# Performance work log

Hardware: AMD Instinct MI355X
Metric: run time of the kernel (lower is better)

## Reference

```python
import jax, jax.numpy as jnp
import numpy as np

N = 100_000
E = 1_000_000
D = 64
NORM_FACTOR = 100.0
LN_EPS = 1e-5


def setup_inputs() -> dict:
    key = jax.random.key(0)
    ks = jax.random.split(key, 8)
    h = jax.random.normal(ks[0], (N, D), dtype=jnp.float32)
    distances = jax.random.uniform(ks[1], (E, 1), dtype=jnp.float32)
    edges = jax.random.randint(ks[2], (2, E), 0, N, dtype=jnp.int64)
    node_mask = jnp.ones((N, 1), dtype=jnp.float32)
    edge_mask = jnp.ones((E, 1), dtype=jnp.float32)
    s = 1.0 / np.sqrt(D)
    W_lin = jax.random.normal(ks[3], (D, D), dtype=jnp.float32) * s
    b_lin = jnp.zeros((D,), dtype=jnp.float32)
    att_W1 = jax.random.normal(ks[4], (D, 2 * D + 1), dtype=jnp.float32) * (1.0 / np.sqrt(2 * D + 1))
    att_b1 = jnp.zeros((D,), dtype=jnp.float32)
    att_W2 = jax.random.normal(ks[5], (1, D), dtype=jnp.float32) * s
    att_b2 = jnp.zeros((1,), dtype=jnp.float32)
    ln_g = jnp.ones((D,), dtype=jnp.float32)
    ln_b = jnp.zeros((D,), dtype=jnp.float32)
    return {"h": h, "distances": distances, "edges": edges, "node_mask": node_mask,
            "edge_mask": edge_mask, "W_lin": W_lin, "b_lin": b_lin,
            "att_W1": att_W1, "att_b1": att_b1, "att_W2": att_W2, "att_b2": att_b2,
            "ln_g": ln_g, "ln_b": ln_b}


def reference(h, distances, edges, node_mask, edge_mask, W_lin, b_lin,
              att_W1, att_b1, att_W2, att_b2, ln_g, ln_b):
    # Linear projection: [N, D]
    x = h @ W_lin.T + b_lin
    row, col = edges[0], edges[1]
    x_row = x[row]          # [E, D]
    x_col = x[col]          # [E, D]
    # DenseAtt: MLP(concat(x_row, x_col, dist)) -> sigmoid -> * edge_mask
    cat = jnp.concatenate([x_row, x_col, distances], axis=1)  # [E, 2D+1]
    hdn = jax.nn.silu(cat @ att_W1.T + att_b1)                # [E, D]
    att = jax.nn.sigmoid(hdn @ att_W2.T + att_b2) * edge_mask # [E, 1]
    # Attention-weighted scatter-sum aggregation into row segments
    agg = x_col * att
    out = jax.ops.segment_sum(agg, row, num_segments=x.shape[0]) / NORM_FACTOR
    out = out + x           # residual
    # LayerNorm + activation
    mu = jnp.mean(out, axis=-1, keepdims=True)
    var = jnp.mean(jnp.square(out - mu), axis=-1, keepdims=True)
    y = (out - mu) * jax.lax.rsqrt(var + LN_EPS) * ln_g + ln_b
    return jax.nn.silu(y)
```

## Files before the change

kernel.cpp:

```cpp
#include <hip/hip_runtime.h>
#include <hip/hip_bf16.h>

#define N_NODES 100000
#define N_EDGES 1000000
#define DIM 64
#define NORM_INV 0.01f
#define LN_EPS 1e-5f
#define N_TILES 6250
#define PROJ_BLOCKS 1563
#define N_BUCKETS 1563
#define HB_PK 784
#define SC_EDGES 4096
#define SC_BLOCKS 245
#define OFS_STRIDE 1568
#define L2E 1.4426950408889634f
#define LN2 0.6931471805599453f
#define CAP 1280

typedef __attribute__((ext_vector_type(8))) short short8;
typedef __attribute__((ext_vector_type(4))) float f32x4;

__device__ __forceinline__ unsigned short f2bf(float f) {
    union { float f; unsigned u; } x; x.f = f;
    unsigned r = x.u + 0x7FFFu + ((x.u >> 16) & 1u);
    return (unsigned short)(r >> 16);
}
__device__ __forceinline__ float bf2f(unsigned short s) {
    union { unsigned u; float f; } x; x.u = ((unsigned)s) << 16; return x.f;
}

__global__ __launch_bounds__(256) void scatter_k(
    const int* __restrict__ edges, const float* __restrict__ dist,
    const float* __restrict__ emask,
    uint2* __restrict__ srec, unsigned short* __restrict__ ofsT) {
    __shared__ __align__(16) char pool[39040];
    __shared__ int wsum[4];
    int* lh = (int*)pool;
    int* lofsP = (int*)pool + HB_PK;
    uint2* lsort = (uint2*)(pool + 6272);
    const int blk = blockIdx.x;
    const int tid = threadIdx.x;
    const int lane = tid & 63;
    const int w = tid >> 6;
    for (int i = tid; i < HB_PK; i += 256) lh[i] = 0;
    __syncthreads();

    const int eb = blk * SC_EDGES;
    const int total = min(SC_EDGES, N_EDGES - eb);

    int rows[16], rank[16];
    uint2 recs[16];
    const int e0 = eb + tid * 16;
#pragma unroll
    for (int g = 0; g < 4; ++g) {
        const int e = e0 + g * 4;
        if (e + 4 <= N_EDGES) {
            const int4 rr = *(const int4*)(edges + e);
            const int4 cc = *(const int4*)(edges + N_EDGES + e);
            const float4 dd = *(const float4*)(dist + e);
            const float4 mm = *(const float4*)(emask + e);
            rows[g*4+0] = rr.x; rows[g*4+1] = rr.y; rows[g*4+2] = rr.z; rows[g*4+3] = rr.w;
            const int c4[4] = {cc.x, cc.y, cc.z, cc.w};
            const float d4[4] = {dd.x, dd.y, dd.z, dd.w};
            const float m4[4] = {mm.x, mm.y, mm.z, mm.w};
#pragma unroll
            for (int i = 0; i < 4; ++i) {
                const int ii = g * 4 + i;
                recs[ii].x = (unsigned)c4[i] | ((unsigned)(rows[ii] & 63) << 24);
                recs[ii].y = (unsigned)f2bf(d4[i]) |
                             ((unsigned)f2bf(m4[i] * NORM_INV) << 16);
                const int bk = rows[ii] >> 6;
                const int sh = (bk & 1) << 4;
                rank[ii] = (atomicAdd(&lh[bk >> 1], 1 << sh) >> sh) & 0xffff;
            }
        } else {
#pragma unroll
            for (int i = 0; i < 4; ++i) {
                const int ii = g * 4 + i;
                const int ee = e + i;
                if (ee < N_EDGES) {
                    rows[ii] = edges[ee];
                    recs[ii].x = (unsigned)edges[N_EDGES + ee] |
                                 ((unsigned)(rows[ii] & 63) << 24);
                    recs[ii].y = (unsigned)f2bf(dist[ee]) |
                                 ((unsigned)f2bf(emask[ee] * NORM_INV) << 16);
                    const int bk = rows[ii] >> 6;
                    const int sh = (bk & 1) << 4;
                    rank[ii] = (atomicAdd(&lh[bk >> 1], 1 << sh) >> sh) & 0xffff;
                } else {
                    rows[ii] = -1;
                }
            }
        }
    }
    __syncthreads();

    const int t4 = tid * 4;
    int li[4];
#pragma unroll
    for (int g = 0; g < 4; ++g) li[g] = (t4 + g < HB_PK) ? lh[t4 + g] : 0;
    int cs[8];
#pragma unroll
    for (int g = 0; g < 4; ++g) {
        cs[2*g]   = li[g] & 0xffff;
        cs[2*g+1] = (li[g] >> 16) & 0xffff;
    }
    int S = 0;
#pragma unroll
    for (int k = 0; k < 8; ++k) S += cs[k];
    int sc = S;
#pragma unroll
    for (int off = 1; off < 64; off <<= 1) {
        int u = __shfl_up(sc, off);
        if (lane >= off) sc += u;
    }
    if (lane == 63) wsum[w] = sc;
    __syncthreads();
    int wbase = 0;
    if (w > 0) wbase = wsum[0];
    if (w > 1) wbase += wsum[1];
    if (w > 2) wbase += wsum[2];
    int run = sc - S + wbase;
#pragma unroll
    for (int g = 0; g < 4; ++g) {
        const int lo = run; run += cs[2*g];
        const int hi = run; run += cs[2*g+1];
        if (t4 + g < HB_PK) lofsP[t4 + g] = (unsigned)lo | ((unsigned)hi << 16);
    }
    __syncthreads();

#pragma unroll
    for (int i = 0; i < 16; ++i) {
        if (rows[i] >= 0) {
            const int bk = rows[i] >> 6;
            const int base = (lofsP[bk >> 1] >> ((bk & 1) << 4)) & 0xffff;
            lsort[base + rank[i]] = recs[i];
        }
    }
    __syncthreads();

    for (int s = tid; s < total; s += 256)
        srec[(size_t)blk * SC_EDGES + s] = lsort[s];
    for (int b = tid; b < 1564; b += 256)
        ofsT[blk * OFS_STRIDE + b] =
            (unsigned short)((lofsP[b >> 1] >> ((b & 1) << 4)) & 0xffff);
}

__global__ __launch_bounds__(256) void proj_k(
    const float* __restrict__ h, const float* __restrict__ bl,
    const float* __restrict__ W, const float* __restrict__ att_W1,
    unsigned short* __restrict__ xv, unsigned short* __restrict__ u_bf) {
    __shared__ __align__(16) char pool[32768];

    const int tid = threadIdx.x;
    const int lane = tid & 63;
    const int wv = tid >> 6;
    const int c = lane & 15, q = lane >> 4;

    {
        short8* Lwhi_w = (short8*)pool;
        short8* Lwlo_w = Lwhi_w + 512;
        short8* Lwa_w  = Lwhi_w + 1024;
        short8* Lwb_w  = Lwhi_w + 1536;
        const int nt_b = tid >> 6;
        const int n_b = nt_b * 16 + c;
#pragma unroll
        for (int ks = 0; ks < 2; ++ks) {
            const int k0 = ks * 32 + q * 8;
            short8 hi8, lo8, a8, b8;
#pragma unroll
            for (int jj = 0; jj < 8; ++jj) {
                float w = W[n_b * 64 + k0 + jj];
                unsigned short hh = f2bf(w);
                hi8[jj] = (short)hh;
                lo8[jj] = (short)f2bf(w - bf2f(hh));
                a8[jj] = (short)f2bf(att_W1[n_b * 129 + k0 + jj]);
                b8[jj] = (short)f2bf(att_W1[n_b * 129 + 64 + k0 + jj]);
            }
            const int idx = (nt_b * 2 + ks) * 64 + lane;
            Lwhi_w[idx] = hi8; Lwlo_w[idx] = lo8; Lwa_w[idx] = a8; Lwb_w[idx] = b8;
        }
    }
    __syncthreads();
    const short8* Lwhi = (const short8*)pool;
    const short8* Lwlo = Lwhi + 512;
    const short8* Lwa  = Lwhi + 1024;
    const short8* Lwb  = Lwhi + 1536;

    const int tile = blockIdx.x * 4 + wv;
    const bool valid = (tile < N_TILES);
    const int n0 = valid ? tile * 16 : 0;

    float bias[4];
#pragma unroll
    for (int nt = 0; nt < 4; ++nt) bias[nt] = bl[nt * 16 + c];

    short8 Ahi[2], Alo[2];
#pragma unroll
    for (int ks = 0; ks < 2; ++ks) {
        const float* hp = h + (size_t)(n0 + c) * 64 + ks * 32 + q * 8;
        f32x4 p0 = *(const f32x4*)hp;
        f32x4 p1 = *(const f32x4*)(hp + 4);
        short8 hi8, lo8;
#pragma unroll
        for (int jj = 0; jj < 4; ++jj) {
            unsigned short hh = f2bf(p0[jj]);
            hi8[jj] = (short)hh; lo8[jj] = (short)f2bf(p0[jj] - bf2f(hh));
            unsigned short h2 = f2bf(p1[jj]);
            hi8[4 + jj] = (short)h2; lo8[4 + jj] = (short)f2bf(p1[jj] - bf2f(h2));
        }
        Ahi[ks] = hi8; Alo[ks] = lo8;
    }

    f32x4 xacc[4] = {{0,0,0,0},{0,0,0,0},{0,0,0,0},{0,0,0,0}};
#pragma unroll
    for (int ks = 0; ks < 2; ++ks)
#pragma unroll
        for (int nt = 0; nt < 4; ++nt) {
            const short8 fhi = Lwhi[(nt * 2 + ks) * 64 + lane];
            const short8 flo = Lwlo[(nt * 2 + ks) * 64 + lane];
            xacc[nt] = __builtin_amdgcn_mfma_f32_16x16x32_bf16(Ahi[ks], fhi, xacc[nt], 0, 0, 0);
            xacc[nt] = __builtin_amdgcn_mfma_f32_16x16x32_bf16(Ahi[ks], flo, xacc[nt], 0, 0, 0);
            xacc[nt] = __builtin_amdgcn_mfma_f32_16x16x32_bf16(Alo[ks], fhi, xacc[nt], 0, 0, 0);
        }

    __syncthreads();

    unsigned short* lw = (unsigned short*)pool + wv * (16 * 72);
    uint2 xpk[4];
#pragma unroll
    for (int r = 0; r < 4; ++r) {
        unsigned short xb[4];
#pragma unroll
        for (int nt = 0; nt < 4; ++nt) {
            unsigned short v16 = f2bf(xacc[nt][r] + bias[nt]);
            xb[nt] = v16;
            lw[(q * 4 + r) * 72 + nt * 16 + c] = v16;
        }
        xpk[r].x = (unsigned)xb[0] | ((unsigned)xb[1] << 16);
        xpk[r].y = (unsigned)xb[2] | ((unsigned)xb[3] << 16);
    }

    short8 Ax[2];
#pragma unroll
    for (int ks = 0; ks < 2; ++ks)
        Ax[ks] = *(const short8*)&lw[c * 72 + ks * 32 + q * 8];

    f32x4 uacc[4] = {{0,0,0,0},{0,0,0,0},{0,0,0,0},{0,0,0,0}};
    f32x4 vacc[4] = {{0,0,0,0},{0,0,0,0},{0,0,0,0},{0,0,0,0}};
#pragma unroll
    for (int ks = 0; ks < 2; ++ks)
#pragma unroll
        for (int nt = 0; nt < 4; ++nt) {
            const short8 fa = Lwa[(nt * 2 + ks) * 64 + lane];
            const short8 fb = Lwb[(nt * 2 + ks) * 64 + lane];
            uacc[nt] = __builtin_amdgcn_mfma_f32_16x16x32_bf16(Ax[ks], fa, uacc[nt], 0, 0, 0);
            vacc[nt] = __builtin_amdgcn_mfma_f32_16x16x32_bf16(Ax[ks], fb, vacc[nt], 0, 0, 0);
        }
    if (valid) {
#pragma unroll
        for (int r = 0; r < 4; ++r) {
            const int node = n0 + q * 4 + r;
            uint2 pu;
            pu.x = (unsigned)f2bf(uacc[0][r] * L2E) | ((unsigned)f2bf(uacc[1][r] * L2E) << 16);
            pu.y = (unsigned)f2bf(uacc[2][r] * L2E) | ((unsigned)f2bf(uacc[3][r] * L2E) << 16);
            *(uint2*)(u_bf + (size_t)node * 64 + c * 4) = pu;
            uint4 pk;
            pk.x = xpk[r].x;
            pk.y = xpk[r].y;
            pk.z = (unsigned)f2bf(vacc[0][r] * L2E) | ((unsigned)f2bf(vacc[1][r] * L2E) << 16);
            pk.w = (unsigned)f2bf(vacc[2][r] * L2E) | ((unsigned)f2bf(vacc[3][r] * L2E) << 16);
            *(uint4*)(xv + (size_t)node * 128 + c * 8) = pk;
        }
    }
}

__global__ __launch_bounds__(256, 8) void agg_fused(
    const uint2* __restrict__ srec, const unsigned short* __restrict__ ofsT,
    const unsigned short* __restrict__ xv, const unsigned short* __restrict__ u_bf,
    const float* __restrict__ att_W1, const float* __restrict__ att_b1,
    const float* __restrict__ att_W2, const float* __restrict__ att_b2,
    const float* __restrict__ ln_g, const float* __restrict__ ln_b,
    float* __restrict__ out) {
    __shared__ __align__(16) uint2 lrecs[CAP + 16];
    __shared__ float4 ltab[64];
    __shared__ int hist[64];
    __shared__ int rst[65];
    __shared__ int cur[64];
    __shared__ int sst[256];
    __shared__ int dbase[257];
    __shared__ int wsum4[4];

    const int b = blockIdx.x;
    const int tid = threadIdx.x;
    const int lane = tid & 63;
    const int wv = tid >> 6;

    if (tid < 64) hist[tid] = 0;
    if (tid >= 192) {
        const int f = tid - 192;
        ltab[f] = make_float4(att_W2[f] * LN2, att_W1[f * 129 + 128] * L2E,
                              att_b1[f] * L2E, 0.f);
    }

    int stv = 0, len = 0, sc0 = 0;
    {
        if (tid < SC_BLOCKS) {
            stv = (int)ofsT[tid * OFS_STRIDE + b];
            len = (int)ofsT[tid * OFS_STRIDE + b + 1] - stv;
        }
        sst[tid] = stv;
        sc0 = len;
#pragma unroll
        for (int off = 1; off < 64; off <<= 1) {
            int u = __shfl_up(sc0, off);
            if (lane >= off) sc0 += u;
        }
        if (lane == 63) wsum4[wv] = sc0;
    }
    __syncthreads();
    {
        int wbase = 0;
        if (wv > 0) wbase = wsum4[0];
        if (wv > 1) wbase += wsum4[1];
        if (wv > 2) wbase += wsum4[2];
        dbase[tid] = wbase + sc0 - len;
        if (tid == 255) dbase[256] = wbase + sc0;
    }
    __syncthreads();
    const int cnt = dbase[245];

    uint2 rec0, rec1, rec2, rec3;
    int lr0 = -1, lr1 = -1, lr2 = -1, lr3 = -1;
#define GATHER(I, RC, LR)                                                     \
    {                                                                         \
        const int m = tid + I * 256;                                          \
        if (m < cnt) {                                                        \
            int lo = 0, hi = 245;                                             \
            while (hi - lo > 1) {                                             \
                const int mid = (lo + hi) >> 1;                               \
                if (dbase[mid] <= m) lo = mid; else hi = mid;                 \
            }                                                                 \
            RC = srec[(size_t)lo * SC_EDGES + sst[lo] + (m - dbase[lo])];     \
            LR = (int)(RC.x >> 24);                                           \
            RC.x &= 0x00FFFFFFu;                                              \
            atomicAdd(&hist[LR], 1);                                          \
        }                                                                     \
    }
    GATHER(0, rec0, lr0)
    GATHER(1, rec1, lr1)
    GATHER(2, rec2, lr2)
    GATHER(3, rec3, lr3)
#undef GATHER
    __syncthreads();

    if (tid < 64) {
        const int c = hist[tid];
        const int p = (c + 3) & ~3;
        int sc = p;
#pragma unroll
        for (int off = 1; off < 64; off <<= 1) {
            int u = __shfl_up(sc, off);
            if (lane >= off) sc += u;
        }
        const int excl = sc - p;
        rst[tid] = excl;
        cur[tid] = excl;
        uint2 z; z.x = 0; z.y = 0;
        for (int i = c; i < p; ++i) lrecs[excl + i] = z;
        if (tid == 63) {
            rst[64] = excl + p;
            for (int i = 0; i < 16; ++i) lrecs[excl + p + i] = z;
        }
    }
    __syncthreads();

    if (lr0 >= 0) lrecs[atomicAdd(&cur[lr0], 1)] = rec0;
    if (lr1 >= 0) lrecs[atomicAdd(&cur[lr1], 1)] = rec1;
    if (lr2 >= 0) lrecs[atomicAdd(&cur[lr2], 1)] = rec2;
    if (lr3 >= 0) lrecs[atomicAdd(&cur[lr3], 1)] = rec3;
    __syncthreads();

    const int j = lane & 15;
    const int sl = lane >> 4;
    const float4 t0 = ltab[j], t1 = ltab[j + 16], t2 = ltab[j + 32], t3 = ltab[j + 48];
    const float b2L = att_b2[0] * L2E;
    const float gg = ln_g[lane], bb = ln_b[lane];
    const unsigned* xvu = (const unsigned*)xv;

#pragma unroll 1
    for (int k = 0; k < 16; ++k) {
        const int lrw = wv + 4 * k;
        const int r = b * 64 + lrw;
        if (r >= N_NODES) break;

        const uint2 uu = *(const uint2*)(u_bf + (size_t)r * 64 + j * 4);
        const float base0 = __uint_as_float(uu.x << 16) + t0.z;
        const float base1 = __uint_as_float(uu.x & 0xffff0000u) + t1.z;
        const float base2 = __uint_as_float(uu.y << 16) + t2.z;
        const float base3 = __uint_as_float(uu.y & 0xffff0000u) + t3.z;

        const int s0 = rst[lrw];
        const int e1 = rst[lrw + 1];

        float a0 = 0.f, a1 = 0.f, a2 = 0.f, a3 = 0.f;
        if (e1 > s0) {
            uint2 recA = lrecs[s0 + sl];
            uint2 recB = lrecs[s0 + 4 + sl];
            uint4 xvA = *(const uint4*)(xvu + (size_t)recA.x * 64 + j * 4);
            uint4 xvB = *(const uint4*)(xvu + (size_t)recB.x * 64 + j * 4);
            for (int e = s0; e < e1; e += 4) {
                const uint2 recC = lrecs[e + 8 + sl];
                const uint4 xvC = *(const uint4*)(xvu + (size_t)recC.x * 64 + j * 4);

                const float dist = __uint_as_float(recA.y << 16);
                const float emN = __uint_as_float(recA.y & 0xffff0000u);
                const float x0 = __uint_as_float(xvA.x << 16);
                const float x1 = __uint_as_float(xvA.x & 0xffff0000u);
                const float x2 = __uint_as_float(xvA.y << 16);
                const float x3 = __uint_as_float(xvA.y & 0xffff0000u);
                const float v0 = __uint_as_float(xvA.z << 16);
                const float v1 = __uint_as_float(xvA.z & 0xffff0000u);
                const float v2 = __uint_as_float(xvA.w << 16);
                const float v3 = __uint_as_float(xvA.w & 0xffff0000u);
                float pv = 0.f, pre, sg;
                pre = fmaf(dist, t0.y, base0) + v0;
                sg = __builtin_amdgcn_rcpf(1.f + __builtin_amdgcn_exp2f(-pre));
                pv = fmaf(pre * sg, t0.x, pv);
                pre = fmaf(dist, t1.y, base1) + v1;
                sg = __builtin_amdgcn_rcpf(1.f + __builtin_amdgcn_exp2f(-pre));
                pv = fmaf(pre * sg, t1.x, pv);
                pre = fmaf(dist, t2.y, base2) + v2;
                sg = __builtin_amdgcn_rcpf(1.f + __builtin_amdgcn_exp2f(-pre));
                pv = fmaf(pre * sg, t2.x, pv);
                pre = fmaf(dist, t3.y, base3) + v3;
                sg = __builtin_amdgcn_rcpf(1.f + __builtin_amdgcn_exp2f(-pre));
                pv = fmaf(pre * sg, t3.x, pv);
                pv += __shfl_xor(pv, 1); pv += __shfl_xor(pv, 2);
                pv += __shfl_xor(pv, 4); pv += __shfl_xor(pv, 8);
                const float sp = fmaf(pv, L2E, b2L);
                const float att =
                    emN * __builtin_amdgcn_rcpf(1.f + __builtin_amdgcn_exp2f(-sp));
                a0 = fmaf(att, x0, a0); a1 = fmaf(att, x1, a1);
                a2 = fmaf(att, x2, a2); a3 = fmaf(att, x3, a3);
                recA = recB; xvA = xvB; recB = recC; xvB = xvC;
            }
        }
        a0 += __shfl_xor(a0, 16); a0 += __shfl_xor(a0, 32);
        a1 += __shfl_xor(a1, 16); a1 += __shfl_xor(a1, 32);
        a2 += __shfl_xor(a2, 16); a2 += __shfl_xor(a2, 32);
        a3 += __shfl_xor(a3, 16); a3 += __shfl_xor(a3, 32);

        const uint2 xr = *(const uint2*)(xvu + (size_t)r * 64 + j * 4);
        const float o0 = __uint_as_float(xr.x << 16) + a0;
        const float o1 = __uint_as_float(xr.x & 0xffff0000u) + a1;
        const float o2 = __uint_as_float(xr.y << 16) + a2;
        const float o3 = __uint_as_float(xr.y & 0xffff0000u) + a3;

        float ssum = o0 + o1 + o2 + o3;
        ssum += __shfl_xor(ssum, 1); ssum += __shfl_xor(ssum, 2);
        ssum += __shfl_xor(ssum, 4); ssum += __shfl_xor(ssum, 8);
        const float mu = ssum * (1.f / 64.f);
        const float d0 = o0 - mu, d1 = o1 - mu, d2 = o2 - mu, d3 = o3 - mu;
        float vs = d0 * d0 + d1 * d1 + d2 * d2 + d3 * d3;
        vs += __shfl_xor(vs, 1); vs += __shfl_xor(vs, 2);
        vs += __shfl_xor(vs, 4); vs += __shfl_xor(vs, 8);
        const float rstd = rsqrtf(vs * (1.f / 64.f) + LN_EPS);

        const float dk = (sl == 0) ? d0 : (sl == 1) ? d1 : (sl == 2) ? d2 : d3;
        const float y = fmaf(dk * rstd, gg, bb);
        out[(size_t)r * 64 + lane] =
            y * __builtin_amdgcn_rcpf(1.f + __builtin_amdgcn_exp2f(-y * L2E));
    }
}

extern "C" void kernel_launch(void* const* d_in, const int* in_sizes, int n_in,
                              void* d_out, int out_size, void* d_ws, size_t ws_size,
                              hipStream_t stream) {
    const float* h      = (const float*)d_in[0];
    const float* dist   = (const float*)d_in[1];
    const int*   edges  = (const int*)d_in[2];
    const float* emask  = (const float*)d_in[4];
    const float* W_lin  = (const float*)d_in[5];
    const float* b_lin  = (const float*)d_in[6];
    const float* att_W1 = (const float*)d_in[7];
    const float* att_b1 = (const float*)d_in[8];
    const float* att_W2 = (const float*)d_in[9];
    const float* att_b2 = (const float*)d_in[10];
    const float* ln_g   = (const float*)d_in[11];
    const float* ln_b   = (const float*)d_in[12];
    float* out = (float*)d_out;

    char* ws = (char*)d_ws;
    unsigned short* xv   = (unsigned short*)ws;
    unsigned short* u_bf = (unsigned short*)(ws + 25600000);
    uint2* srec          = (uint2*)(ws + 38400000);
    unsigned short* ofsT = (unsigned short*)(ws + 46428160);

    scatter_k<<<SC_BLOCKS, 256, 0, stream>>>(edges, dist, emask, srec, ofsT);
    proj_k<<<PROJ_BLOCKS, 256, 0, stream>>>(h, b_lin, W_lin, att_W1, xv, u_bf);
    agg_fused<<<N_BUCKETS, 256, 0, stream>>>(srec, ofsT, xv, u_bf,
                                             att_W1, att_b1, att_W2, att_b2,
                                             ln_g, ln_b, out);
}
```

Baseline: 197.2 us.

## Merge scatter and projection into one launch and split aggregation launch

```diff
diff --git a/kernel.cpp b/kernel.cpp
--- a/kernel.cpp
+++ b/kernel.cpp
@@ -9,6 +9,8 @@
 #define N_TILES 6250
 #define PROJ_BLOCKS 1563
 #define N_BUCKETS 1563
+#define AGG_C0 782
+#define AGG_C1 781
 #define HB_PK 784
 #define SC_EDGES 4096
 #define SC_BLOCKS 245
@@ -29,128 +31,128 @@
     union { unsigned u; float f; } x; x.u = ((unsigned)s) << 16; return x.f;
 }
 
-__global__ __launch_bounds__(256) void scatter_k(
+__global__ __launch_bounds__(256) void proj_scatter(
+    const float* __restrict__ h, const float* __restrict__ bl,
+    const float* __restrict__ W, const float* __restrict__ att_W1,
     const int* __restrict__ edges, const float* __restrict__ dist,
     const float* __restrict__ emask,
-    uint2* __restrict__ srec, unsigned short* __restrict__ ofsT) {
-    __shared__ __align__(16) char pool[39040];
+    uint2* __restrict__ srec, unsigned short* __restrict__ ofsT,
+    unsigned short* __restrict__ xv, unsigned short* __restrict__ u_bf) {
+    __shared__ __align__(16) char pool[39168];
     __shared__ int wsum[4];
-    int* lh = (int*)pool;
-    int* lofsP = (int*)pool + HB_PK;
-    uint2* lsort = (uint2*)(pool + 6272);
-    const int blk = blockIdx.x;
-    const int tid = threadIdx.x;
-    const int lane = tid & 63;
-    const int w = tid >> 6;
-    for (int i = tid; i < HB_PK; i += 256) lh[i] = 0;
-    __syncthreads();
-
-    const int eb = blk * SC_EDGES;
-    const int total = min(SC_EDGES, N_EDGES - eb);
-
-    int rows[16], rank[16];
-    uint2 recs[16];
-    const int e0 = eb + tid * 16;
-#pragma unroll
-    for (int g = 0; g < 4; ++g) {
-        const int e = e0 + g * 4;
-        if (e + 4 <= N_EDGES) {
-            const int4 rr = *(const int4*)(edges + e);
-            const int4 cc = *(const int4*)(edges + N_EDGES + e);
-            const float4 dd = *(const float4*)(dist + e);
-            const float4 mm = *(const float4*)(emask + e);
-            rows[g*4+0] = rr.x; rows[g*4+1] = rr.y; rows[g*4+2] = rr.z; rows[g*4+3] = rr.w;
-            const int c4[4] = {cc.x, cc.y, cc.z, cc.w};
-            const float d4[4] = {dd.x, dd.y, dd.z, dd.w};
-            const float m4[4] = {mm.x, mm.y, mm.z, mm.w};
-#pragma unroll
-            for (int i = 0; i < 4; ++i) {
-                const int ii = g * 4 + i;
-                recs[ii].x = (unsigned)c4[i] | ((unsigned)(rows[ii] & 63) << 24);
-                recs[ii].y = (unsigned)f2bf(d4[i]) |
-                             ((unsigned)f2bf(m4[i] * NORM_INV) << 16);
-                const int bk = rows[ii] >> 6;
-                const int sh = (bk & 1) << 4;
-                rank[ii] = (atomicAdd(&lh[bk >> 1], 1 << sh) >> sh) & 0xffff;
-            }
-        } else {
-#pragma unroll
-            for (int i = 0; i < 4; ++i) {
-                const int ii = g * 4 + i;
-                const int ee = e + i;
-                if (ee < N_EDGES) {
-                    rows[ii] = edges[ee];
-                    recs[ii].x = (unsigned)edges[N_EDGES + ee] |
-                                 ((unsigned)(rows[ii] & 63) << 24);
-                    recs[ii].y = (unsigned)f2bf(dist[ee]) |
-                                 ((unsigned)f2bf(emask[ee] * NORM_INV) << 16);
+
+    if (blockIdx.x < SC_BLOCKS) {
+        int* lh = (int*)pool;
+        int* lofsP = (int*)pool + HB_PK;
+        uint2* lsort = (uint2*)(pool + 6272);
+        const int blk = blockIdx.x;
+        const int tid = threadIdx.x;
+        const int lane = tid & 63;
+        const int w = tid >> 6;
+        for (int i = tid; i < HB_PK; i += 256) lh[i] = 0;
+        __syncthreads();
+
+        const int eb = blk * SC_EDGES;
+        const int total = min(SC_EDGES, N_EDGES - eb);
+
+        int rows[16], rank[16];
+        uint2 recs[16];
+        const int e0 = eb + tid * 16;
+#pragma unroll
+        for (int g = 0; g < 4; ++g) {
+            const int e = e0 + g * 4;
+            if (e + 4 <= N_EDGES) {
+                const int4 rr = *(const int4*)(edges + e);
+                const int4 cc = *(const int4*)(edges + N_EDGES + e);
+                const float4 dd = *(const float4*)(dist + e);
+                const float4 mm = *(const float4*)(emask + e);
+                rows[g*4+0] = rr.x; rows[g*4+1] = rr.y; rows[g*4+2] = rr.z; rows[g*4+3] = rr.w;
+                const int c4[4] = {cc.x, cc.y, cc.z, cc.w};
+                const float d4[4] = {dd.x, dd.y, dd.z, dd.w};
+                const float m4[4] = {mm.x, mm.y, mm.z, mm.w};
+#pragma unroll
+                for (int i = 0; i < 4; ++i) {
+                    const int ii = g * 4 + i;
+                    recs[ii].x = (unsigned)c4[i] | ((unsigned)(rows[ii] & 63) << 24);
+                    recs[ii].y = (unsigned)f2bf(d4[i]) |
+                                 ((unsigned)f2bf(m4[i] * NORM_INV) << 16);
                     const int bk = rows[ii] >> 6;
                     const int sh = (bk & 1) << 4;
                     rank[ii] = (atomicAdd(&lh[bk >> 1], 1 << sh) >> sh) & 0xffff;
-                } else {
-                    rows[ii] = -1;
+                }
+            } else {
+#pragma unroll
+                for (int i = 0; i < 4; ++i) {
+                    const int ii = g * 4 + i;
+                    const int ee = e + i;
+                    if (ee < N_EDGES) {
+                        rows[ii] = edges[ee];
+                        recs[ii].x = (unsigned)edges[N_EDGES + ee] |
+                                     ((unsigned)(rows[ii] & 63) << 24);
+                        recs[ii].y = (unsigned)f2bf(dist[ee]) |
+                                     ((unsigned)f2bf(emask[ee] * NORM_INV) << 16);
+                        const int bk = rows[ii] >> 6;
+                        const int sh = (bk & 1) << 4;
+                        rank[ii] = (atomicAdd(&lh[bk >> 1], 1 << sh) >> sh) & 0xffff;
+                    } else {
+                        rows[ii] = -1;
+                    }
                 }
             }
         }
-    }
-    __syncthreads();
-
-    const int t4 = tid * 4;
-    int li[4];
-#pragma unroll
-    for (int g = 0; g < 4; ++g) li[g] = (t4 + g < HB_PK) ? lh[t4 + g] : 0;
-    int cs[8];
-#pragma unroll
-    for (int g = 0; g < 4; ++g) {
-        cs[2*g]   = li[g] & 0xffff;
-        cs[2*g+1] = (li[g] >> 16) & 0xffff;
-    }
-    int S = 0;
-#pragma unroll
-    for (int k = 0; k < 8; ++k) S += cs[k];
-    int sc = S;
-#pragma unroll
-    for (int off = 1; off < 64; off <<= 1) {
-        int u = __shfl_up(sc, off);
-        if (lane >= off) sc += u;
-    }
-    if (lane == 63) wsum[w] = sc;
-    __syncthreads();
-    int wbase = 0;
-    if (w > 0) wbase = wsum[0];
-    if (w > 1) wbase += wsum[1];
-    if (w > 2) wbase += wsum[2];
-    int run = sc - S + wbase;
-#pragma unroll
-    for (int g = 0; g < 4; ++g) {
-        const int lo = run; run += cs[2*g];
-        const int hi = run; run += cs[2*g+1];
-        if (t4 + g < HB_PK) lofsP[t4 + g] = (unsigned)lo | ((unsigned)hi << 16);
-    }
-    __syncthreads();
-
-#pragma unroll
-    for (int i = 0; i < 16; ++i) {
-        if (rows[i] >= 0) {
-            const int bk = rows[i] >> 6;
-            const int base = (lofsP[bk >> 1] >> ((bk & 1) << 4)) & 0xffff;
-            lsort[base + rank[i]] = recs[i];
-        }
-    }
-    __syncthreads();
-
-    for (int s = tid; s < total; s += 256)
-        srec[(size_t)blk * SC_EDGES + s] = lsort[s];
-    for (int b = tid; b < 1564; b += 256)
-        ofsT[blk * OFS_STRIDE + b] =
-            (unsigned short)((lofsP[b >> 1] >> ((b & 1) << 4)) & 0xffff);
-}
-
-__global__ __launch_bounds__(256) void proj_k(
-    const float* __restrict__ h, const float* __restrict__ bl,
-    const float* __restrict__ W, const float* __restrict__ att_W1,
-    unsigned short* __restrict__ xv, unsigned short* __restrict__ u_bf) {
-    __shared__ __align__(16) char pool[32768];
+        __syncthreads();
+
+        const int t4 = tid * 4;
+        int li[4];
+#pragma unroll
+        for (int g = 0; g < 4; ++g) li[g] = (t4 + g < HB_PK) ? lh[t4 + g] : 0;
+        int cs[8];
+#pragma unroll
+        for (int g = 0; g < 4; ++g) {
+            cs[2*g]   = li[g] & 0xffff;
+            cs[2*g+1] = (li[g] >> 16) & 0xffff;
+        }
+        int S = 0;
+#pragma unroll
+        for (int k = 0; k < 8; ++k) S += cs[k];
+        int sc = S;
+#pragma unroll
+        for (int off = 1; off < 64; off <<= 1) {
+            int u = __shfl_up(sc, off);
+            if (lane >= off) sc += u;
+        }
+        if (lane == 63) wsum[w] = sc;
+        __syncthreads();
+        int wbase = 0;
+        if (w > 0) wbase = wsum[0];
+        if (w > 1) wbase += wsum[1];
+        if (w > 2) wbase += wsum[2];
+        int run = sc - S + wbase;
+#pragma unroll
+        for (int g = 0; g < 4; ++g) {
+            const int lo = run; run += cs[2*g];
+            const int hi = run; run += cs[2*g+1];
+            if (t4 + g < HB_PK) lofsP[t4 + g] = (unsigned)lo | ((unsigned)hi << 16);
+        }
+        __syncthreads();
+
+#pragma unroll
+        for (int i = 0; i < 16; ++i) {
+            if (rows[i] >= 0) {
+                const int bk = rows[i] >> 6;
+                const int base = (lofsP[bk >> 1] >> ((bk & 1) << 4)) & 0xffff;
+                lsort[base + rank[i]] = recs[i];
+            }
+        }
+        __syncthreads();
+
+        for (int s = tid; s < total; s += 256)
+            srec[(size_t)blk * SC_EDGES + s] = lsort[s];
+        for (int b = tid; b < 1564; b += 256)
+            ofsT[blk * OFS_STRIDE + b] =
+                (unsigned short)((lofsP[b >> 1] >> ((b & 1) << 4)) & 0xffff);
+        return;
+    }
 
     const int tid = threadIdx.x;
     const int lane = tid & 63;
@@ -187,7 +189,7 @@
     const short8* Lwa  = Lwhi + 1024;
     const short8* Lwb  = Lwhi + 1536;
 
-    const int tile = blockIdx.x * 4 + wv;
+    const int tile = (blockIdx.x - SC_BLOCKS) * 4 + wv;
     const bool valid = (tile < N_TILES);
     const int n0 = valid ? tile * 16 : 0;
 
@@ -281,7 +283,7 @@
     const float* __restrict__ att_W1, const float* __restrict__ att_b1,
     const float* __restrict__ att_W2, const float* __restrict__ att_b2,
     const float* __restrict__ ln_g, const float* __restrict__ ln_b,
-    float* __restrict__ out) {
+    float* __restrict__ out, const int bbase) {
     __shared__ __align__(16) uint2 lrecs[CAP + 16];
     __shared__ float4 ltab[64];
     __shared__ int hist[64];
@@ -291,7 +293,7 @@
     __shared__ int dbase[257];
     __shared__ int wsum4[4];
 
-    const int b = blockIdx.x;
+    const int b = bbase + blockIdx.x;
     const int tid = threadIdx.x;
     const int lane = tid & 63;
     const int wv = tid >> 6;
@@ -413,7 +415,7 @@
                 const uint2 recC = lrecs[e + 8 + sl];
                 const uint4 xvC = *(const uint4*)(xvu + (size_t)recC.x * 64 + j * 4);
 
-                const float dist = __uint_as_float(recA.y << 16);
+                const float dst = __uint_as_float(recA.y << 16);
                 const float emN = __uint_as_float(recA.y & 0xffff0000u);
                 const float x0 = __uint_as_float(xvA.x << 16);
                 const float x1 = __uint_as_float(xvA.x & 0xffff0000u);
@@ -424,16 +426,16 @@
                 const float v2 = __uint_as_float(xvA.w << 16);
                 const float v3 = __uint_as_float(xvA.w & 0xffff0000u);
                 float pv = 0.f, pre, sg;
-                pre = fmaf(dist, t0.y, base0) + v0;
+                pre = fmaf(dst, t0.y, base0) + v0;
                 sg = __builtin_amdgcn_rcpf(1.f + __builtin_amdgcn_exp2f(-pre));
                 pv = fmaf(pre * sg, t0.x, pv);
-                pre = fmaf(dist, t1.y, base1) + v1;
+                pre = fmaf(dst, t1.y, base1) + v1;
                 sg = __builtin_amdgcn_rcpf(1.f + __builtin_amdgcn_exp2f(-pre));
                 pv = fmaf(pre * sg, t1.x, pv);
-                pre = fmaf(dist, t2.y, base2) + v2;
+                pre = fmaf(dst, t2.y, base2) + v2;
                 sg = __builtin_amdgcn_rcpf(1.f + __builtin_amdgcn_exp2f(-pre));
                 pv = fmaf(pre * sg, t2.x, pv);
-                pre = fmaf(dist, t3.y, base3) + v3;
+                pre = fmaf(dst, t3.y, base3) + v3;
                 sg = __builtin_amdgcn_rcpf(1.f + __builtin_amdgcn_exp2f(-pre));
                 pv = fmaf(pre * sg, t3.x, pv);
                 pv += __shfl_xor(pv, 1); pv += __shfl_xor(pv, 2);
@@ -497,9 +499,12 @@
     uint2* srec          = (uint2*)(ws + 38400000);
     unsigned short* ofsT = (unsigned short*)(ws + 46428160);
 
-    scatter_k<<<SC_BLOCKS, 256, 0, stream>>>(edges, dist, emask, srec, ofsT);
-    proj_k<<<PROJ_BLOCKS, 256, 0, stream>>>(h, b_lin, W_lin, att_W1, xv, u_bf);
-    agg_fused<<<N_BUCKETS, 256, 0, stream>>>(srec, ofsT, xv, u_bf,
-                                             att_W1, att_b1, att_W2, att_b2,
-                                             ln_g, ln_b, out);
+    proj_scatter<<<SC_BLOCKS + PROJ_BLOCKS, 256, 0, stream>>>(
+        h, b_lin, W_lin, att_W1, edges, dist, emask, srec, ofsT, xv, u_bf);
+    agg_fused<<<AGG_C0, 256, 0, stream>>>(srec, ofsT, xv, u_bf,
+                                          att_W1, att_b1, att_W2, att_b2,
+                                          ln_g, ln_b, out, 0);
+    agg_fused<<<AGG_C1, 256, 0, stream>>>(srec, ofsT, xv, u_bf,
+                                          att_W1, att_b1, att_W2, att_b2,
+                                          ln_g, ln_b, out, AGG_C0);
 }
```

Result: slower. 233.1 us (+18.2%).
